# Optimization experiments

Measured on AMD Instinct MI355X. Metric: run time of the kernel, lower is better.

## Reference

```python
import jax, jax.numpy as jnp
import numpy as np

S, B, H = 4096, 32, 512

def setup_inputs() -> dict:
    key = jax.random.key(0)
    k1, k2, k3, k4, k5 = jax.random.split(key, 5)
    hidden = jax.random.normal(k1, (1, B, H), dtype=jnp.float32)
    encoder_outputs = jax.random.normal(k2, (S, B, H), dtype=jnp.float32)
    embedding = jax.random.normal(k3, (S, B, 3), dtype=jnp.float32)
    # learned params (xavier-ish scale)
    bigram_matrix = jax.random.normal(k4, (H, H), dtype=jnp.float32) * (1.0 / np.sqrt(H))
    affect_matrix = jax.random.normal(k5, (H, 3), dtype=jnp.float32) * 0.1
    return {"hidden": hidden, "encoder_outputs": encoder_outputs,
            "embedding": embedding, "bigram_matrix": bigram_matrix,
            "affect_matrix": affect_matrix}

def reference(hidden, encoder_outputs, embedding, bigram_matrix, affect_matrix):
    # hidden: [1,B,H] -> [B,H] (view(-1) over single layer)
    h = hidden[0]
    # bigram-modulated encoder states:
    #   i == 0: enc[0]
    #   i  > 0: (enc[i-1] @ W_bigram) * enc[i]
    modulated = jnp.einsum('sbh,hk->sbk', encoder_outputs[:-1], bigram_matrix) * encoder_outputs[1:]
    bigram_hidden = jnp.concatenate([encoder_outputs[:1], modulated], axis=0)  # [S,B,H]
    # dot-attention energy per (b, s)
    e_dot = jnp.einsum('sbh,bh->bs', bigram_hidden, h)  # [B,S]
    # affect term: (h @ affect_matrix) . embedding[s,b]
    e_aff = jnp.einsum('bk,sbk->bs', jnp.einsum('bh,hk->bk', h, affect_matrix), embedding)
    attn = jax.nn.softmax(e_dot + e_aff, axis=-1)  # softmax over seq dim
    return attn[:, None, :]  # [B,1,S]
```

## Files before the change

kernel.cpp:

```cpp
#include <hip/hip_runtime.h>
#include <cstdint>
#include <cstddef>

#define S_DIM 4096
#define B_DIM 32
#define H_DIM 512
#define M_DIM (S_DIM * B_DIM)

typedef unsigned short u16;
typedef unsigned int u32;
typedef float f32x4 __attribute__((ext_vector_type(4)));
typedef __bf16 bf16x8 __attribute__((ext_vector_type(8)));

__device__ __forceinline__ u16 f2bf(float v) {
    union { float f; u32 u; } a; a.f = v;
    u32 r = a.u + 0x7fffu + ((a.u >> 16) & 1u);
    return (u16)(r >> 16);
}
__device__ __forceinline__ float bf2f(u16 b) {
    union { float f; u32 u; } a; a.u = ((u32)b) << 16; return a.f;
}
__device__ __forceinline__ void split_bf(float v, u16& h, u16& l) {
    h = f2bf(v);
    l = f2bf(v - bf2f(h));
}

__device__ __forceinline__ void gl2lds16(const void* g, void* l) {
    __builtin_amdgcn_global_load_lds(
        (const __attribute__((address_space(1))) unsigned int*)g,
        (__attribute__((address_space(3))) unsigned int*)l,
        16, 0, 0);
}

__global__ void prep_w(const float* __restrict__ W,
                       u16* __restrict__ Wh, u16* __restrict__ Wl) {
    int i = blockIdx.x * 256 + threadIdx.x;
    float w = W[i];
    u16 h, l;
    split_bf(w, h, l);
    Wh[i] = h; Wl[i] = l;
}

__device__ __forceinline__ void split4_store(
    float4 e, float4 h, u16* dh, u16* dl)
{
    float vf[4] = { e.x * h.x, e.y * h.y, e.z * h.z, e.w * h.w };
    u32 rh[4], rl[4];
    #pragma unroll
    for (int i = 0; i < 4; ++i) {
        const u32 u = __float_as_uint(vf[i]);
        rh[i] = (u + 0x7fffu + ((u >> 16) & 1u)) & 0xffff0000u;
        const float lo_f = vf[i] - __uint_as_float(rh[i]);
        const u32 ul = __float_as_uint(lo_f);
        rl[i] = ul + 0x7fffu + ((ul >> 16) & 1u);
    }
    uint2 hw, lw;
    hw.x = rh[1] | (rh[0] >> 16);
    hw.y = rh[3] | (rh[2] >> 16);
    lw.x = (rl[1] & 0xffff0000u) | (rl[0] >> 16);
    lw.y = (rl[3] & 0xffff0000u) | (rl[2] >> 16);
    *(uint2*)dh = hw;
    *(uint2*)dl = lw;
}

__global__ __launch_bounds__(256, 3) void bigram_gemm_fused(
    const float* __restrict__ enc,
    const float* __restrict__ hid,
    const u16* __restrict__ Wh, const u16* __restrict__ Wl,
    float* __restrict__ Lp)
{
    __shared__ u16 sAh[128 * 32];
    __shared__ u16 sAl[128 * 32];
    __shared__ u16 sBh[2][128 * 32];
    __shared__ u16 sBl[2][128 * 32];
    __shared__ float rowsum[2][128];

    const int tid  = threadIdx.x;
    const int wave = tid >> 6;
    const int lane = tid & 63;
    const int wr   = wave >> 1;
    const int wc   = wave & 1;
    const int logical = (blockIdx.x & 7) * 512 + (blockIdx.x >> 3);
    const int jt   = logical & 3;
    const int mt   = logical >> 2;
    const int m0   = mt * 128;
    const int j0   = jt * 128;
    const int g    = lane >> 4;
    const int cl   = lane & 15;

    const int srow = wave * 32 + (lane >> 2);
    const int scol = (lane & 3) * 8;
    const size_t boff0 = (size_t)(j0 + srow) * H_DIM + scol;
    const size_t boff1 = boff0 + (size_t)16 * H_DIM;
    const u16* pBh0 = Wh + boff0; const u16* pBh1 = Wh + boff1;
    const u16* pBl0 = Wl + boff0; const u16* pBl1 = Wl + boff1;
    const int d0 = wave * 1024, d1 = d0 + 512;

    const int abrow = tid >> 3;
    const int akq   = tid & 7;
    const float* pe0 = enc + (size_t)(m0 +  0 + abrow) * H_DIM + akq * 4;
    const float* pe1 = enc + (size_t)(m0 + 32 + abrow) * H_DIM + akq * 4;
    const float* pe2 = enc + (size_t)(m0 + 64 + abrow) * H_DIM + akq * 4;
    const float* pe3 = enc + (size_t)(m0 + 96 + abrow) * H_DIM + akq * 4;
    const float* ph  = hid + (size_t)abrow * H_DIM + akq * 4;
    const int awoff = abrow * 32 + akq * 4;

    f32x4 acc[4][4];
    #pragma unroll
    for (int mf = 0; mf < 4; ++mf)
        #pragma unroll
        for (int nf = 0; nf < 4; ++nf)
            acc[mf][nf] = (f32x4){0.f, 0.f, 0.f, 0.f};

    float4 e0 = *(const float4*)pe0;
    float4 e1 = *(const float4*)pe1;
    float4 e2 = *(const float4*)pe2;
    float4 e3 = *(const float4*)pe3;
    float4 eh = *(const float4*)ph;
    gl2lds16(pBh0, &sBh[0][d0]);
    gl2lds16(pBh1, &sBh[0][d1]);
    gl2lds16(pBl0, &sBl[0][d0]);
    gl2lds16(pBl1, &sBl[0][d1]);
    split4_store(e0, eh, sAh + 0 * 1024 + awoff, sAl + 0 * 1024 + awoff);
    split4_store(e1, eh, sAh + 1 * 1024 + awoff, sAl + 1 * 1024 + awoff);
    split4_store(e2, eh, sAh + 2 * 1024 + awoff, sAl + 2 * 1024 + awoff);
    split4_store(e3, eh, sAh + 3 * 1024 + awoff, sAl + 3 * 1024 + awoff);
    e0 = *(const float4*)(pe0 + 32);
    e1 = *(const float4*)(pe1 + 32);
    e2 = *(const float4*)(pe2 + 32);
    e3 = *(const float4*)(pe3 + 32);
    eh = *(const float4*)(ph + 32);
    __syncthreads();

#define GEMM_ITER(KT, CUR)                                                     \
  {                                                                            \
    bf16x8 ah[4], al[4];                                                       \
    _Pragma("unroll")                                                          \
    for (int mf = 0; mf < 4; ++mf) {                                           \
      const int ar = wr * 64 + mf * 16 + cl;                                   \
      ah[mf] = *(const bf16x8*)(sAh + ar * 32 + g * 8);                        \
      al[mf] = *(const bf16x8*)(sAl + ar * 32 + g * 8);                        \
    }                                                                          \
    __syncthreads();  \
    if ((KT) < 15) {                                                           \
      const int ko = ((KT) + 1) * 32;                                          \
      gl2lds16(pBh0 + ko, &sBh[(CUR) ^ 1][d0]);                                \
      gl2lds16(pBh1 + ko, &sBh[(CUR) ^ 1][d1]);                                \
      gl2lds16(pBl0 + ko, &sBl[(CUR) ^ 1][d0]);                                \
      gl2lds16(pBl1 + ko, &sBl[(CUR) ^ 1][d1]);                                \
      split4_store(e0, eh, sAh + 0 * 1024 + awoff, sAl + 0 * 1024 + awoff);    \
      split4_store(e1, eh, sAh + 1 * 1024 + awoff, sAl + 1 * 1024 + awoff);    \
      split4_store(e2, eh, sAh + 2 * 1024 + awoff, sAl + 2 * 1024 + awoff);    \
      split4_store(e3, eh, sAh + 3 * 1024 + awoff, sAl + 3 * 1024 + awoff);    \
    }                                                                          \
    if ((KT) < 14) {                                                           \
      const int ko2 = ((KT) + 2) * 32;                                         \
      e0 = *(const float4*)(pe0 + ko2);                                        \
      e1 = *(const float4*)(pe1 + ko2);                                        \
      e2 = *(const float4*)(pe2 + ko2);                                        \
      e3 = *(const float4*)(pe3 + ko2);                                        \
      eh = *(const float4*)(ph + ko2);                                         \
    }                                                                          \
    _Pragma("unroll")                                                          \
    for (int nf = 0; nf < 4; ++nf) {                                           \
      const int br = wc * 64 + nf * 16 + cl;                                   \
      const bf16x8 bh = *(const bf16x8*)(&sBh[(CUR)][br * 32 + g * 8]);        \
      const bf16x8 bl = *(const bf16x8*)(&sBl[(CUR)][br * 32 + g * 8]);        \
      _Pragma("unroll")                                                        \
      for (int mf = 0; mf < 4; ++mf) {                                         \
        acc[mf][nf] = __builtin_amdgcn_mfma_f32_16x16x32_bf16(ah[mf], bh, acc[mf][nf], 0, 0, 0); \
        acc[mf][nf] = __builtin_amdgcn_mfma_f32_16x16x32_bf16(ah[mf], bl, acc[mf][nf], 0, 0, 0); \
        acc[mf][nf] = __builtin_amdgcn_mfma_f32_16x16x32_bf16(al[mf], bh, acc[mf][nf], 0, 0, 0); \
      }                                                                        \
    }                                                                          \
    __syncthreads();    \
  }

    for (int kt = 0; kt < 16; kt += 2) {
        GEMM_ITER(kt, 0);
        GEMM_ITER(kt + 1, 1);
    }
#undef GEMM_ITER

    #pragma unroll
    for (int mf = 0; mf < 4; ++mf) {
        float rs0 = 0.f, rs1 = 0.f, rs2 = 0.f, rs3 = 0.f;
        const int growb = m0 + wr * 64 + mf * 16 + g * 4;
        #pragma unroll
        for (int nf = 0; nf < 4; ++nf) {
            const int gcol = j0 + wc * 64 + nf * 16 + cl;
            float ee0 = (growb + 0 >= B_DIM) ? enc[(size_t)(growb + 0 - B_DIM) * H_DIM + gcol] : 0.f;
            float ee1 = (growb + 1 >= B_DIM) ? enc[(size_t)(growb + 1 - B_DIM) * H_DIM + gcol] : 0.f;
            float ee2 = (growb + 2 >= B_DIM) ? enc[(size_t)(growb + 2 - B_DIM) * H_DIM + gcol] : 0.f;
            float ee3 = (growb + 3 >= B_DIM) ? enc[(size_t)(growb + 3 - B_DIM) * H_DIM + gcol] : 0.f;
            rs0 += acc[mf][nf][0] * ee0;
            rs1 += acc[mf][nf][1] * ee1;
            rs2 += acc[mf][nf][2] * ee2;
            rs3 += acc[mf][nf][3] * ee3;
        }
        #pragma unroll
        for (int off = 1; off < 16; off <<= 1) {
            rs0 += __shfl_xor(rs0, off);
            rs1 += __shfl_xor(rs1, off);
            rs2 += __shfl_xor(rs2, off);
            rs3 += __shfl_xor(rs3, off);
        }
        if (cl == 0) {
            const int rb = wr * 64 + mf * 16 + g * 4;
            rowsum[wc][rb + 0] = rs0;
            rowsum[wc][rb + 1] = rs1;
            rowsum[wc][rb + 2] = rs2;
            rowsum[wc][rb + 3] = rs3;
        }
    }
    __syncthreads();
    if (tid < 128) {
        const int gm = m0 + tid;
        if (gm >= B_DIM) {
            Lp[(size_t)jt * M_DIM + (size_t)(gm & 31) * S_DIM + (gm >> 5)] =
                rowsum[0][tid] + rowsum[1][tid];
        }
    }
}

__global__ __launch_bounds__(256) void prep_aff(
    const float* __restrict__ enc,
    const float* __restrict__ hid,
    const float* __restrict__ aff,
    float* __restrict__ Aux)
{
    __shared__ float w[4][4];
    const int b    = blockIdx.x;
    const int tid  = threadIdx.x;
    const int wave = tid >> 6;
    const int lane = tid & 63;

    float p0 = 0.f, p1 = 0.f, p2 = 0.f, p3 = 0.f;
    #pragma unroll
    for (int it = 0; it < 2; ++it) {
        const int h = tid + it * 256;
        const float hv = hid[b * H_DIM + h];
        p0 += hv * aff[h * 3 + 0];
        p1 += hv * aff[h * 3 + 1];
        p2 += hv * aff[h * 3 + 2];
        p3 += hv * enc[(size_t)b * H_DIM + h];
    }
    #pragma unroll
    for (int off = 32; off > 0; off >>= 1) {
        p0 += __shfl_xor(p0, off);
        p1 += __shfl_xor(p1, off);
        p2 += __shfl_xor(p2, off);
        p3 += __shfl_xor(p3, off);
    }
    if (lane == 0) { w[wave][0] = p0; w[wave][1] = p1; w[wave][2] = p2; w[wave][3] = p3; }
    __syncthreads();
    if (tid < 4)
        Aux[b * 4 + tid] = w[0][tid] + w[1][tid] + w[2][tid] + w[3][tid];
}

__global__ __launch_bounds__(256) void sm_partial(
    const float* __restrict__ emb,
    const float* __restrict__ Lp,
    const float* __restrict__ Aux,
    float* __restrict__ Lg,
    float* __restrict__ Part)
{
    __shared__ float wm[4];
    __shared__ float wsum[4];
    const int b     = blockIdx.x >> 3;
    const int strip = blockIdx.x & 7;
    const int tid   = threadIdx.x;
    const int wave  = tid >> 6;
    const int lane  = tid & 63;

    const float ha0 = Aux[b * 4 + 0], ha1 = Aux[b * 4 + 1],
                ha2 = Aux[b * 4 + 2], s0dot = Aux[b * 4 + 3];

    float lgv[2];
    float mx = -3.4e38f;
    #pragma unroll
    for (int it = 0; it < 2; ++it) {
        const int s = strip * 512 + it * 256 + tid;
        const size_t base = (size_t)b * S_DIM + s;
        const float ed = (s == 0) ? s0dot
            : (Lp[base] + Lp[(size_t)M_DIM + base] + Lp[2 * (size_t)M_DIM + base] + Lp[3 * (size_t)M_DIM + base]);
        const float* e = emb + (size_t)(s * B_DIM + b) * 3;
        const float lg = ed + ha0 * e[0] + ha1 * e[1] + ha2 * e[2];
        Lg[(size_t)b * S_DIM + s] = lg;
        lgv[it] = lg;
        mx = fmaxf(mx, lg);
    }
    #pragma unroll
    for (int off = 32; off > 0; off >>= 1) mx = fmaxf(mx, __shfl_xor(mx, off));
    if (lane == 0) wm[wave] = mx;
    __syncthreads();
    mx = fmaxf(fmaxf(wm[0], wm[1]), fmaxf(wm[2], wm[3]));

    float sum = __expf(lgv[0] - mx) + __expf(lgv[1] - mx);
    #pragma unroll
    for (int off = 32; off > 0; off >>= 1) sum += __shfl_xor(sum, off);
    if (lane == 0) wsum[wave] = sum;
    __syncthreads();
    if (tid == 0) {
        Part[(size_t)(b * 8 + strip) * 2 + 0] = mx;
        Part[(size_t)(b * 8 + strip) * 2 + 1] = wsum[0] + wsum[1] + wsum[2] + wsum[3];
    }
}

__global__ __launch_bounds__(256) void sm_final(
    const float* __restrict__ Lg,
    const float* __restrict__ Part,
    float* __restrict__ out)
{
    const int b     = blockIdx.x >> 3;
    const int strip = blockIdx.x & 7;
    const int tid   = threadIdx.x;

    float M = -3.4e38f;
    #pragma unroll
    for (int i = 0; i < 8; ++i) M = fmaxf(M, Part[(size_t)(b * 8 + i) * 2]);
    float S = 0.f;
    #pragma unroll
    for (int i = 0; i < 8; ++i)
        S += Part[(size_t)(b * 8 + i) * 2 + 1] * __expf(Part[(size_t)(b * 8 + i) * 2] - M);
    const float inv = 1.0f / S;

    #pragma unroll
    for (int it = 0; it < 2; ++it) {
        const int s = strip * 512 + it * 256 + tid;
        out[(size_t)b * S_DIM + s] = __expf(Lg[(size_t)b * S_DIM + s] - M) * inv;
    }
}

extern "C" void kernel_launch(void* const* d_in, const int* in_sizes, int n_in,
                              void* d_out, int out_size, void* d_ws, size_t ws_size,
                              hipStream_t stream) {
    const float* hid = (const float*)d_in[0];
    const float* enc = (const float*)d_in[1];
    const float* emb = (const float*)d_in[2];
    const float* Wm  = (const float*)d_in[3];
    const float* aff = (const float*)d_in[4];
    float* out = (float*)d_out;

    char* ws = (char*)d_ws;
    u16*   Wh  = (u16*)ws;
    u16*   Wl  = (u16*)(ws + (512u << 10));
    float* Lp  = (float*)(ws + (1024u << 10));
    float* Aux = (float*)(ws + (3072u << 10));
    float* Lg  = (float*)(ws + (3072u << 10) + 1024);
    float* Part= (float*)(ws + (3072u << 10) + 1024 + (512u << 10));

    hipLaunchKernelGGL(prep_w, dim3(1024), dim3(256), 0, stream, Wm, Wh, Wl);
    hipLaunchKernelGGL(prep_aff, dim3(32), dim3(256), 0, stream, enc, hid, aff, Aux);
    hipLaunchKernelGGL(bigram_gemm_fused, dim3(4096), dim3(256), 0, stream,
                       enc, hid, Wh, Wl, Lp);
    hipLaunchKernelGGL(sm_partial, dim3(256), dim3(256), 0, stream,
                       emb, Lp, Aux, Lg, Part);
    hipLaunchKernelGGL(sm_final, dim3(256), dim3(256), 0, stream,
                       Lg, Part, out);
}
```

Baseline: 558.5 us.

## Load GEMM operands directly from global into registers, bypassing LDS staging

Rewrites the main bigram GEMM so each wave loads its encoder rows and W tiles straight from global memory into MFMA fragment registers instead of staging them through shared memory with barriers. The bf16 hi/lo split of the encoder×hidden product now uses byte-permute truncation rather than round-to-nearest, and register double buffering of the encoder rows replaces the LDS double buffer. The goal is to remove LDS traffic and __syncthreads overhead. In exchange, operands shared between waves are now loaded redundantly from global/L2, register pressure rises (launch bounds lowered to 2 blocks per SIMD), and truncation slightly changes numerics.

```diff
diff --git a/kernel.cpp b/kernel.cpp
--- a/kernel.cpp
+++ b/kernel.cpp
@@ -10,6 +10,7 @@
 typedef unsigned short u16;
 typedef unsigned int u32;
 typedef float f32x4 __attribute__((ext_vector_type(4)));
+typedef float f32x8 __attribute__((ext_vector_type(8)));
 typedef __bf16 bf16x8 __attribute__((ext_vector_type(8)));
 
 __device__ __forceinline__ u16 f2bf(float v) {
@@ -23,13 +24,6 @@
 __device__ __forceinline__ void split_bf(float v, u16& h, u16& l) {
     h = f2bf(v);
     l = f2bf(v - bf2f(h));
-}
-
-__device__ __forceinline__ void gl2lds16(const void* g, void* l) {
-    __builtin_amdgcn_global_load_lds(
-        (const __attribute__((address_space(1))) unsigned int*)g,
-        (__attribute__((address_space(3))) unsigned int*)l,
-        16, 0, 0);
 }
 
 __global__ void prep_w(const float* __restrict__ W,
@@ -41,38 +35,32 @@
     Wh[i] = h; Wl[i] = l;
 }
 
-__device__ __forceinline__ void split4_store(
-    float4 e, float4 h, u16* dh, u16* dl)
-{
-    float vf[4] = { e.x * h.x, e.y * h.y, e.z * h.z, e.w * h.w };
-    u32 rh[4], rl[4];
-    #pragma unroll
-    for (int i = 0; i < 4; ++i) {
-        const u32 u = __float_as_uint(vf[i]);
-        rh[i] = (u + 0x7fffu + ((u >> 16) & 1u)) & 0xffff0000u;
-        const float lo_f = vf[i] - __uint_as_float(rh[i]);
-        const u32 ul = __float_as_uint(lo_f);
-        rl[i] = ul + 0x7fffu + ((ul >> 16) & 1u);
-    }
-    uint2 hw, lw;
-    hw.x = rh[1] | (rh[0] >> 16);
-    hw.y = rh[3] | (rh[2] >> 16);
-    lw.x = (rl[1] & 0xffff0000u) | (rl[0] >> 16);
-    lw.y = (rl[3] & 0xffff0000u) | (rl[2] >> 16);
-    *(uint2*)dh = hw;
-    *(uint2*)dl = lw;
-}
-
-__global__ __launch_bounds__(256, 3) void bigram_gemm_fused(
+union Bf8u { bf16x8 v; u32 w[4]; };
+
+__device__ __forceinline__ bf16x8 pack_hi8(const f32x8& v) {
+    Bf8u r;
+    #pragma unroll
+    for (int j = 0; j < 4; ++j)
+        r.w[j] = __builtin_amdgcn_perm(
+            __float_as_uint(v[2 * j + 1]),
+            __float_as_uint(v[2 * j]),
+            0x07060302u);
+    return r.v;
+}
+__device__ __forceinline__ f32x8 trunc_residual(const f32x8& v) {
+    f32x8 lo;
+    #pragma unroll
+    for (int j = 0; j < 8; ++j)
+        lo[j] = v[j] - __uint_as_float(__float_as_uint(v[j]) & 0xffff0000u);
+    return lo;
+}
+
+__global__ __launch_bounds__(256, 2) void bigram_gemm_direct2(
     const float* __restrict__ enc,
     const float* __restrict__ hid,
     const u16* __restrict__ Wh, const u16* __restrict__ Wl,
     float* __restrict__ Lp)
 {
-    __shared__ u16 sAh[128 * 32];
-    __shared__ u16 sAl[128 * 32];
-    __shared__ u16 sBh[2][128 * 32];
-    __shared__ u16 sBl[2][128 * 32];
     __shared__ float rowsum[2][128];
 
     const int tid  = threadIdx.x;
@@ -88,22 +76,20 @@
     const int g    = lane >> 4;
     const int cl   = lane & 15;
 
-    const int srow = wave * 32 + (lane >> 2);
-    const int scol = (lane & 3) * 8;
-    const size_t boff0 = (size_t)(j0 + srow) * H_DIM + scol;
-    const size_t boff1 = boff0 + (size_t)16 * H_DIM;
-    const u16* pBh0 = Wh + boff0; const u16* pBh1 = Wh + boff1;
-    const u16* pBl0 = Wl + boff0; const u16* pBl1 = Wl + boff1;
-    const int d0 = wave * 1024, d1 = d0 + 512;
-
-    const int abrow = tid >> 3;
-    const int akq   = tid & 7;
-    const float* pe0 = enc + (size_t)(m0 +  0 + abrow) * H_DIM + akq * 4;
-    const float* pe1 = enc + (size_t)(m0 + 32 + abrow) * H_DIM + akq * 4;
-    const float* pe2 = enc + (size_t)(m0 + 64 + abrow) * H_DIM + akq * 4;
-    const float* pe3 = enc + (size_t)(m0 + 96 + abrow) * H_DIM + akq * 4;
-    const float* ph  = hid + (size_t)abrow * H_DIM + akq * 4;
-    const int awoff = abrow * 32 + akq * 4;
+    const float* pe0 = enc + (size_t)(m0 + wr * 64 +  0 + cl) * H_DIM + g * 8;
+    const float* pe1 = enc + (size_t)(m0 + wr * 64 + 16 + cl) * H_DIM + g * 8;
+    const float* pe2 = enc + (size_t)(m0 + wr * 64 + 32 + cl) * H_DIM + g * 8;
+    const float* pe3 = enc + (size_t)(m0 + wr * 64 + 48 + cl) * H_DIM + g * 8;
+    const float* ph0 = hid + (size_t)cl * H_DIM + g * 8;
+    const float* ph1 = hid + (size_t)(cl + 16) * H_DIM + g * 8;
+    const u16* pbh0 = Wh + (size_t)(j0 + wc * 64 +  0 + cl) * H_DIM + g * 8;
+    const u16* pbh1 = Wh + (size_t)(j0 + wc * 64 + 16 + cl) * H_DIM + g * 8;
+    const u16* pbh2 = Wh + (size_t)(j0 + wc * 64 + 32 + cl) * H_DIM + g * 8;
+    const u16* pbh3 = Wh + (size_t)(j0 + wc * 64 + 48 + cl) * H_DIM + g * 8;
+    const u16* pbl0 = Wl + (size_t)(j0 + wc * 64 +  0 + cl) * H_DIM + g * 8;
+    const u16* pbl1 = Wl + (size_t)(j0 + wc * 64 + 16 + cl) * H_DIM + g * 8;
+    const u16* pbl2 = Wl + (size_t)(j0 + wc * 64 + 32 + cl) * H_DIM + g * 8;
+    const u16* pbl3 = Wl + (size_t)(j0 + wc * 64 + 48 + cl) * H_DIM + g * 8;
 
     f32x4 acc[4][4];
     #pragma unroll
@@ -112,75 +98,61 @@
         for (int nf = 0; nf < 4; ++nf)
             acc[mf][nf] = (f32x4){0.f, 0.f, 0.f, 0.f};
 
-    float4 e0 = *(const float4*)pe0;
-    float4 e1 = *(const float4*)pe1;
-    float4 e2 = *(const float4*)pe2;
-    float4 e3 = *(const float4*)pe3;
-    float4 eh = *(const float4*)ph;
-    gl2lds16(pBh0, &sBh[0][d0]);
-    gl2lds16(pBh1, &sBh[0][d1]);
-    gl2lds16(pBl0, &sBl[0][d0]);
-    gl2lds16(pBl1, &sBl[0][d1]);
-    split4_store(e0, eh, sAh + 0 * 1024 + awoff, sAl + 0 * 1024 + awoff);
-    split4_store(e1, eh, sAh + 1 * 1024 + awoff, sAl + 1 * 1024 + awoff);
-    split4_store(e2, eh, sAh + 2 * 1024 + awoff, sAl + 2 * 1024 + awoff);
-    split4_store(e3, eh, sAh + 3 * 1024 + awoff, sAl + 3 * 1024 + awoff);
-    e0 = *(const float4*)(pe0 + 32);
-    e1 = *(const float4*)(pe1 + 32);
-    e2 = *(const float4*)(pe2 + 32);
-    e3 = *(const float4*)(pe3 + 32);
-    eh = *(const float4*)(ph + 32);
-    __syncthreads();
-
-#define GEMM_ITER(KT, CUR)                                                     \
+    f32x8 xa0 = *(const f32x8*)(pe0);
+    f32x8 xa1 = *(const f32x8*)(pe1);
+    f32x8 xa2 = *(const f32x8*)(pe2);
+    f32x8 xa3 = *(const f32x8*)(pe3);
+    f32x8 xb0, xb1, xb2, xb3;
+
+#define COMPUTE(E0, E1, E2, E3, KT)                                            \
   {                                                                            \
+    const int ko = (KT) * 32;                                                  \
+    const f32x8 h0 = *(const f32x8*)(ph0 + ko);                                \
+    const f32x8 h1 = *(const f32x8*)(ph1 + ko);                                \
     bf16x8 ah[4], al[4];                                                       \
-    _Pragma("unroll")                                                          \
-    for (int mf = 0; mf < 4; ++mf) {                                           \
-      const int ar = wr * 64 + mf * 16 + cl;                                   \
-      ah[mf] = *(const bf16x8*)(sAh + ar * 32 + g * 8);                        \
-      al[mf] = *(const bf16x8*)(sAl + ar * 32 + g * 8);                        \
+    {                                                                          \
+      f32x8 v;                                                                 \
+      v = E0 * h0; ah[0] = pack_hi8(v); al[0] = pack_hi8(trunc_residual(v));   \
+      v = E1 * h1; ah[1] = pack_hi8(v); al[1] = pack_hi8(trunc_residual(v));   \
+      v = E2 * h0; ah[2] = pack_hi8(v); al[2] = pack_hi8(trunc_residual(v));   \
+      v = E3 * h1; ah[3] = pack_hi8(v); al[3] = pack_hi8(trunc_residual(v));   \
     }                                                                          \
-    __syncthreads();  \
-    if ((KT) < 15) {                                                           \
-      const int ko = ((KT) + 1) * 32;                                          \
-      gl2lds16(pBh0 + ko, &sBh[(CUR) ^ 1][d0]);                                \
-      gl2lds16(pBh1 + ko, &sBh[(CUR) ^ 1][d1]);                                \
-      gl2lds16(pBl0 + ko, &sBl[(CUR) ^ 1][d0]);                                \
-      gl2lds16(pBl1 + ko, &sBl[(CUR) ^ 1][d1]);                                \
-      split4_store(e0, eh, sAh + 0 * 1024 + awoff, sAl + 0 * 1024 + awoff);    \
-      split4_store(e1, eh, sAh + 1 * 1024 + awoff, sAl + 1 * 1024 + awoff);    \
-      split4_store(e2, eh, sAh + 2 * 1024 + awoff, sAl + 2 * 1024 + awoff);    \
-      split4_store(e3, eh, sAh + 3 * 1024 + awoff, sAl + 3 * 1024 + awoff);    \
-    }                                                                          \
-    if ((KT) < 14) {                                                           \
-      const int ko2 = ((KT) + 2) * 32;                                         \
-      e0 = *(const float4*)(pe0 + ko2);                                        \
-      e1 = *(const float4*)(pe1 + ko2);                                        \
-      e2 = *(const float4*)(pe2 + ko2);                                        \
-      e3 = *(const float4*)(pe3 + ko2);                                        \
-      eh = *(const float4*)(ph + ko2);                                         \
-    }                                                                          \
+    bf16x8 bh[4], bl[4];                                                       \
+    bh[0] = *(const bf16x8*)(pbh0 + ko); bl[0] = *(const bf16x8*)(pbl0 + ko);  \
+    bh[1] = *(const bf16x8*)(pbh1 + ko); bl[1] = *(const bf16x8*)(pbl1 + ko);  \
+    bh[2] = *(const bf16x8*)(pbh2 + ko); bl[2] = *(const bf16x8*)(pbl2 + ko);  \
+    bh[3] = *(const bf16x8*)(pbh3 + ko); bl[3] = *(const bf16x8*)(pbl3 + ko);  \
     _Pragma("unroll")                                                          \
     for (int nf = 0; nf < 4; ++nf) {                                           \
-      const int br = wc * 64 + nf * 16 + cl;                                   \
-      const bf16x8 bh = *(const bf16x8*)(&sBh[(CUR)][br * 32 + g * 8]);        \
-      const bf16x8 bl = *(const bf16x8*)(&sBl[(CUR)][br * 32 + g * 8]);        \
       _Pragma("unroll")                                                        \
       for (int mf = 0; mf < 4; ++mf) {                                         \
-        acc[mf][nf] = __builtin_amdgcn_mfma_f32_16x16x32_bf16(ah[mf], bh, acc[mf][nf], 0, 0, 0); \
-        acc[mf][nf] = __builtin_amdgcn_mfma_f32_16x16x32_bf16(ah[mf], bl, acc[mf][nf], 0, 0, 0); \
-        acc[mf][nf] = __builtin_amdgcn_mfma_f32_16x16x32_bf16(al[mf], bh, acc[mf][nf], 0, 0, 0); \
+        acc[mf][nf] = __builtin_amdgcn_mfma_f32_16x16x32_bf16(ah[mf], bh[nf], acc[mf][nf], 0, 0, 0); \
+        acc[mf][nf] = __builtin_amdgcn_mfma_f32_16x16x32_bf16(ah[mf], bl[nf], acc[mf][nf], 0, 0, 0); \
+        acc[mf][nf] = __builtin_amdgcn_mfma_f32_16x16x32_bf16(al[mf], bh[nf], acc[mf][nf], 0, 0, 0); \
       }                                                                        \
     }                                                                          \
-    __syncthreads();    \
   }
 
+    #pragma unroll 1
     for (int kt = 0; kt < 16; kt += 2) {
-        GEMM_ITER(kt, 0);
-        GEMM_ITER(kt + 1, 1);
-    }
-#undef GEMM_ITER
+        {
+            const int ko = (kt + 1) * 32;
+            xb0 = *(const f32x8*)(pe0 + ko);
+            xb1 = *(const f32x8*)(pe1 + ko);
+            xb2 = *(const f32x8*)(pe2 + ko);
+            xb3 = *(const f32x8*)(pe3 + ko);
+        }
+        COMPUTE(xa0, xa1, xa2, xa3, kt);
+        if (kt + 2 < 16) {
+            const int ko = (kt + 2) * 32;
+            xa0 = *(const f32x8*)(pe0 + ko);
+            xa1 = *(const f32x8*)(pe1 + ko);
+            xa2 = *(const f32x8*)(pe2 + ko);
+            xa3 = *(const f32x8*)(pe3 + ko);
+        }
+        COMPUTE(xb0, xb1, xb2, xb3, kt + 1);
+    }
+#undef COMPUTE
 
     #pragma unroll
     for (int mf = 0; mf < 4; ++mf) {
@@ -352,7 +324,7 @@
 
     hipLaunchKernelGGL(prep_w, dim3(1024), dim3(256), 0, stream, Wm, Wh, Wl);
     hipLaunchKernelGGL(prep_aff, dim3(32), dim3(256), 0, stream, enc, hid, aff, Aux);
-    hipLaunchKernelGGL(bigram_gemm_fused, dim3(4096), dim3(256), 0, stream,
+    hipLaunchKernelGGL(bigram_gemm_direct2, dim3(4096), dim3(256), 0, stream,
                        enc, hid, Wh, Wl, Lp);
     hipLaunchKernelGGL(sm_partial, dim3(256), dim3(256), 0, stream,
                        emb, Lp, Aux, Lg, Part);
```

Measured after the change: 869.3 us. 1.56x slower.
